# Kernel tuning notes

Measured on AMD Instinct MI355X. Metric: run time of the kernel, lower is better.

## Reference

```python
import jax, jax.numpy as jnp
import numpy as np

H = 64  # LSTM hidden size
IN = 5  # input feature size
N_ACTIONS = 3


def _init_params(key):
    ks = jax.random.split(key, 16)
    def u(k, shape, fan_in):
        b = 1.0 / np.sqrt(fan_in)
        return jax.random.uniform(k, shape, jnp.float32, -b, b)
    p = {}
    # PyTorch LSTM params: gate order i, f, g, o stacked along dim 0
    p['W_ih'] = u(ks[0], (4 * H, IN), H)
    p['W_hh'] = u(ks[1], (4 * H, H), H)
    p['b_ih'] = u(ks[2], (4 * H,), H)
    p['b_hh'] = u(ks[3], (4 * H,), H)
    p['W1'] = u(ks[4], (256, 64), 64); p['b1'] = u(ks[5], (256,), 64)
    p['W2'] = u(ks[6], (64, 256), 256); p['b2'] = u(ks[7], (64,), 256)
    p['W3'] = u(ks[8], (32, 64), 64); p['b3'] = u(ks[9], (32,), 64)
    p['W4'] = u(ks[10], (16, 32), 32); p['b4'] = u(ks[11], (16,), 32)
    p['Wh'] = u(ks[12], (N_ACTIONS, 16), 16); p['bh'] = u(ks[13], (N_ACTIONS,), 16)
    return p


def setup_inputs() -> dict:
    key = jax.random.key(0)
    k_x, k_h, k_c, k_p = jax.random.split(key, 4)
    B = 262144
    inp = {
        'x': jax.random.normal(k_x, (2, B, IN), jnp.float32),
        'h0': jax.random.normal(k_h, (B, H), jnp.float32),
        'c0': jax.random.normal(k_c, (B, H), jnp.float32),
    }
    inp.update(_init_params(k_p))
    return inp


def _lstm_step(x_t, h, c, W_ih, W_hh, b_ih, b_hh):
    # gates: [B, 4H], PyTorch order i, f, g, o
    gates = x_t @ W_ih.T + h @ W_hh.T + (b_ih + b_hh)
    i, f, g, o = jnp.split(gates, 4, axis=-1)
    i = jax.nn.sigmoid(i)
    f = jax.nn.sigmoid(f)
    g = jnp.tanh(g)
    o = jax.nn.sigmoid(o)
    c = f * c + i * g
    h = o * jnp.tanh(c)
    return h, c


def reference(x, h0, c0, W_ih, W_hh, b_ih, b_hh, W1, b1, W2, b2, W3, b3, W4, b4, Wh, bh):
    # 2-step LSTM (seq_len hard-coded to 2 in the torch module)
    h, c = h0, c0
    for t in range(2):
        h, c = _lstm_step(x[t], h, c, W_ih, W_hh, b_ih, b_hh)
    # take last timestep output, relu, then 4-layer MLP + head
    z = jax.nn.relu(h)
    z = jax.nn.relu(z @ W1.T + b1)
    z = jax.nn.relu(z @ W2.T + b2)
    z = jax.nn.relu(z @ W3.T + b3)
    z = jax.nn.relu(z @ W4.T + b4)
    return z @ Wh.T + bh
```

## Files before the change

kernel.cpp:

```cpp
#include <hip/hip_runtime.h>

typedef _Float16 f16;
typedef _Float16 f16x4 __attribute__((ext_vector_type(4)));
typedef _Float16 f16x8 __attribute__((ext_vector_type(8)));
typedef float    f32x4 __attribute__((ext_vector_type(4)));

__device__ __forceinline__ float sigmf(float x) {
    return __builtin_amdgcn_rcpf(1.0f + __expf(-x));
}
__device__ __forceinline__ float tanhf_fast(float x) {
    return 2.0f * sigmf(2.0f * x) - 1.0f;
}
#define MFMA(A,B,C) __builtin_amdgcn_mfma_f32_16x16x32_f16((A),(B),(C),0,0,0)

constexpr int STR = 72;

__global__ __launch_bounds__(512, 2)
void lstmdqn_v5(const float* __restrict__ xg,  const float* __restrict__ h0g,
                const float* __restrict__ c0g,
                const float* __restrict__ Wih, const float* __restrict__ Whh,
                const float* __restrict__ bih, const float* __restrict__ bhh,
                const float* __restrict__ w1p, const float* __restrict__ b1p,
                const float* __restrict__ w2p, const float* __restrict__ b2p,
                const float* __restrict__ w3p, const float* __restrict__ b3p,
                const float* __restrict__ w4p, const float* __restrict__ b4p,
                const float* __restrict__ whp, const float* __restrict__ bhp,
                float* __restrict__ out, int Bsz, int nt32) {
    __shared__ f16 sAB[256 * STR];
    __shared__ f16 sWG[9 * 256 * 8];
    __shared__ f16 sW1[8 * 256 * 8];
    __shared__ f16 sW2[32 * 64 * 8];
    __shared__ f16 sW3[8 * 32 * 8];
    __shared__ f16 sW4[4 * 16 * 8];
    __shared__ f16 sWh[4 * 16 * 8];
    __shared__ f16 sZL[2560];

    const int tid  = threadIdx.x;
    const int w    = tid >> 6, l = tid & 63;
    const int lrow = l & 15, hi = l >> 4;
    const int wrow = w * 32;

    for (int idx = tid; idx < 9 * 256 * 8; idx += 512) {
        int s = idx >> 11, n = (idx >> 3) & 255, j = idx & 7;
        float v;
        if (s < 8) v = Whh[n * 64 + s * 8 + j];
        else       v = (j < 5) ? Wih[n * 5 + j] : (j == 5 ? bih[n] + bhh[n] : 0.0f);
        sWG[idx] = (f16)v;
    }
    for (int idx = tid; idx < 8 * 256 * 8; idx += 512) {
        int s = idx >> 11, n = (idx >> 3) & 255, j = idx & 7;
        sW1[idx] = (f16)w1p[n * 64 + s * 8 + j];
    }
    for (int idx = tid; idx < 32 * 64 * 8; idx += 512) {
        int s = idx >> 9, n = (idx >> 3) & 63, j = idx & 7;
        sW2[idx] = (f16)w2p[n * 256 + s * 8 + j];
    }
    for (int idx = tid; idx < 8 * 32 * 8; idx += 512) {
        int s = idx >> 8, n = (idx >> 3) & 31, j = idx & 7;
        sW3[idx] = (f16)w3p[n * 64 + s * 8 + j];
    }
    for (int idx = tid; idx < 4 * 16 * 8; idx += 512) {
        int s = idx >> 7, n = (idx >> 3) & 15, j = idx & 7;
        sW4[idx] = (f16)w4p[n * 32 + s * 8 + j];
        int k = s * 8 + j;
        sWh[idx] = (f16)((k < 16 && n < 3) ? whp[n * 16 + k] : 0.0f);
    }
    for (int idx = tid; idx < 2560; idx += 512) sZL[idx] = (f16)0.0f;
    for (int idx = tid; idx < 256 * 3; idx += 512) {
        int r = idx / 3, c = 69 + (idx - 3 * r);
        sAB[r * STR + c] = (f16)(c == 69 ? 1.0f : 0.0f);
    }
    float bz1[16], bz2[4], bz3[2], bz4, bzh;
    #pragma unroll
    for (int ct = 0; ct < 16; ++ct) bz1[ct] = b1p[ct * 16 + lrow];
    #pragma unroll
    for (int ct = 0; ct < 4; ++ct)  bz2[ct] = b2p[ct * 16 + lrow];
    bz3[0] = b3p[lrow]; bz3[1] = b3p[16 + lrow];
    bz4 = b4p[lrow];
    bzh = (lrow < 3) ? bhp[lrow] : 0.0f;
    __syncthreads();

    const f16* pA[2]  = { &sAB[(wrow +  0 + lrow) * STR + hi * 8],
                          &sAB[(wrow + 16 + lrow) * STR + hi * 8] };
    const f16* pA2[2] = { (hi == 0) ? &sAB[(wrow +  0 + lrow) * STR + 64] : &sZL[l * 8],
                          (hi == 0) ? &sAB[(wrow + 16 + lrow) * STR + 64] : &sZL[l * 8] };
    const f16* pWG  = &sWG[(hi * 256 + lrow) * 8];
    const f16* pWG2 = (hi == 0) ? &sWG[8 * 2048 + lrow * 8] : &sZL[l * 8];
    const f16* pW1  = &sW1[(hi * 256 + lrow) * 8];
    const f16* pW2  = &sW2[(hi * 64 + lrow) * 8];
    const f16* pW3  = &sW3[(hi * 32 + lrow) * 8];
    const f16* pW4  = &sW4[(hi * 16 + lrow) * 8];
    const f16* pWh  = &sWh[(hi * 16 + lrow) * 8];
    int rowW[2][4];
    #pragma unroll
    for (int s = 0; s < 2; ++s)
        #pragma unroll
        for (int q = 0; q < 4; ++q)
            rowW[s][q] = (wrow + 16 * s + 4 * hi + q) * STR + lrow;

    #pragma unroll 1
    for (int tile = blockIdx.x * 8 + w; tile < nt32; tile += (gridDim.x << 3)) {
        const int rbase = tile * 32;

        {
            const float* hp = h0g + (size_t)rbase * 64;
            #pragma unroll
            for (int e = 0; e < 8; ++e) {
                float4 v = *(const float4*)(hp + e * 256 + l * 4);
                int r = wrow + 4 * e + (l >> 4);
                int col = (4 * l) & 63;
                f16x4 hv = { (f16)v.x, (f16)v.y, (f16)v.z, (f16)v.w };
                *(f16x4*)&sAB[r * STR + col] = hv;
            }
        }
        float creg[2][4][4];
        #pragma unroll
        for (int s = 0; s < 2; ++s)
            #pragma unroll
            for (int cg = 0; cg < 4; ++cg)
                #pragma unroll
                for (int q = 0; q < 4; ++q)
                    creg[s][cg][q] = c0g[(size_t)(rbase + 16 * s + 4 * hi + q) * 64 + cg * 16 + lrow];

        #pragma unroll
        for (int t = 0; t < 2; ++t) {
            if (l < 40) {
                const float* xp = xg + (size_t)t * Bsz * 5 + (size_t)rbase * 5;
                float4 v = *(const float4*)(xp + 4 * l);
                float vv[4] = { v.x, v.y, v.z, v.w };
                #pragma unroll
                for (int e = 0; e < 4; ++e) {
                    int idx = 4 * l + e, r = idx / 5, ft = idx - 5 * r;
                    sAB[(wrow + r) * STR + 64 + ft] = (f16)vv[e];
                }
            }
            f16x8 af0[2], af1[2], af2[2];
            #pragma unroll
            for (int s = 0; s < 2; ++s) {
                af0[s] = *(const f16x8*)&pA[s][0];
                af1[s] = *(const f16x8*)&pA[s][32];
                af2[s] = *(const f16x8*)pA2[s];
            }
            f32x4 acc[2][16];
            #pragma unroll
            for (int ct = 0; ct < 16; ++ct) {
                f16x8 b0 = *(const f16x8*)&pWG[ct * 128];
                f16x8 b1 = *(const f16x8*)&pWG[8192 + ct * 128];
                f16x8 b2 = *(const f16x8*)&pWG2[ct * 128];
                #pragma unroll
                for (int s = 0; s < 2; ++s) {
                    f32x4 a = { 0.f, 0.f, 0.f, 0.f };
                    a = MFMA(af0[s], b0, a);
                    a = MFMA(af1[s], b1, a);
                    a = MFMA(af2[s], b2, a);
                    acc[s][ct] = a;
                }
            }
            #pragma unroll
            for (int s = 0; s < 2; ++s)
                #pragma unroll
                for (int cg = 0; cg < 4; ++cg)
                    #pragma unroll
                    for (int q = 0; q < 4; ++q) {
                        float iv = sigmf(acc[s][cg][q]);
                        float fv = sigmf(acc[s][4 + cg][q]);
                        float gv = tanhf_fast(acc[s][8 + cg][q]);
                        float ov = sigmf(acc[s][12 + cg][q]);
                        float c  = fv * creg[s][cg][q] + iv * gv;
                        creg[s][cg][q] = c;
                        float h = ov * tanhf_fast(c);
                        if (t == 1) h = fmaxf(h, 0.0f);
                        sAB[rowW[s][q] + cg * 16] = (f16)h;
                    }
        }

        f16x8 za[2][2];
        #pragma unroll
        for (int s = 0; s < 2; ++s) {
            za[s][0] = *(const f16x8*)&pA[s][0];
            za[s][1] = *(const f16x8*)&pA[s][32];
        }
        f32x4 acc1[2][16];
        #pragma unroll
        for (int ct = 0; ct < 16; ++ct) {
            f16x8 b0 = *(const f16x8*)&pW1[ct * 128];
            f16x8 b1 = *(const f16x8*)&pW1[8192 + ct * 128];
            #pragma unroll
            for (int s = 0; s < 2; ++s) {
                f32x4 a = { 0.f, 0.f, 0.f, 0.f };
                a = MFMA(za[s][0], b0, a);
                a = MFMA(za[s][1], b1, a);
                acc1[s][ct] = a;
            }
        }
        f32x4 acc2[2][4];
        #pragma unroll
        for (int s = 0; s < 2; ++s)
            #pragma unroll
            for (int ct = 0; ct < 4; ++ct)
                acc2[s][ct] = (f32x4){ 0.f, 0.f, 0.f, 0.f };
        #pragma unroll
        for (int cc = 0; cc < 4; ++cc) {
            #pragma unroll
            for (int s = 0; s < 2; ++s)
                #pragma unroll
                for (int ctl = 0; ctl < 4; ++ctl)
                    #pragma unroll
                    for (int q = 0; q < 4; ++q) {
                        float v = fmaxf(acc1[s][cc * 4 + ctl][q] + bz1[cc * 4 + ctl], 0.0f);
                        sAB[rowW[s][q] + ctl * 16] = (f16)v;
                    }
            f16x8 ca[2][2];
            #pragma unroll
            for (int s = 0; s < 2; ++s) {
                ca[s][0] = *(const f16x8*)&pA[s][0];
                ca[s][1] = *(const f16x8*)&pA[s][32];
            }
            #pragma unroll
            for (int ct2 = 0; ct2 < 4; ++ct2) {
                f16x8 bb0 = *(const f16x8*)&pW2[cc * 4096 + ct2 * 128];
                f16x8 bb1 = *(const f16x8*)&pW2[cc * 4096 + 2048 + ct2 * 128];
                #pragma unroll
                for (int s = 0; s < 2; ++s) {
                    acc2[s][ct2] = MFMA(ca[s][0], bb0, acc2[s][ct2]);
                    acc2[s][ct2] = MFMA(ca[s][1], bb1, acc2[s][ct2]);
                }
            }
        }
        #pragma unroll
        for (int s = 0; s < 2; ++s)
            #pragma unroll
            for (int ct2 = 0; ct2 < 4; ++ct2)
                #pragma unroll
                for (int q = 0; q < 4; ++q) {
                    float v = fmaxf(acc2[s][ct2][q] + bz2[ct2], 0.0f);
                    sAB[rowW[s][q] + ct2 * 16] = (f16)v;
                }
        {
            f16x8 a3[2][2];
            #pragma unroll
            for (int s = 0; s < 2; ++s) {
                a3[s][0] = *(const f16x8*)&pA[s][0];
                a3[s][1] = *(const f16x8*)&pA[s][32];
            }
            f32x4 acc3[2][2];
            #pragma unroll
            for (int ctt = 0; ctt < 2; ++ctt) {
                f16x8 c0f = *(const f16x8*)&pW3[ctt * 128];
                f16x8 c1f = *(const f16x8*)&pW3[1024 + ctt * 128];
                #pragma unroll
                for (int s = 0; s < 2; ++s) {
                    f32x4 a = { 0.f, 0.f, 0.f, 0.f };
                    a = MFMA(a3[s][0], c0f, a);
                    a = MFMA(a3[s][1], c1f, a);
                    acc3[s][ctt] = a;
                }
            }
            #pragma unroll
            for (int s = 0; s < 2; ++s)
                #pragma unroll
                for (int ctt = 0; ctt < 2; ++ctt)
                    #pragma unroll
                    for (int q = 0; q < 4; ++q) {
                        float v = fmaxf(acc3[s][ctt][q] + bz3[ctt], 0.0f);
                        sAB[rowW[s][q] + ctt * 16] = (f16)v;
                    }
        }
        {
            f16x8 wb4 = *(const f16x8*)pW4;
            f32x4 acc4[2];
            #pragma unroll
            for (int s = 0; s < 2; ++s) {
                f16x8 a4 = *(const f16x8*)&pA[s][0];
                f32x4 a = { 0.f, 0.f, 0.f, 0.f };
                acc4[s] = MFMA(a4, wb4, a);
            }
            #pragma unroll
            for (int s = 0; s < 2; ++s)
                #pragma unroll
                for (int q = 0; q < 4; ++q) {
                    float v = fmaxf(acc4[s][q] + bz4, 0.0f);
                    sAB[rowW[s][q] + 32] = (f16)v;
                }
        }
        {
            f16x8 wbh = *(const f16x8*)pWh;
            f32x4 acch[2];
            #pragma unroll
            for (int s = 0; s < 2; ++s) {
                f16x8 ah = *(const f16x8*)&pA[s][32];
                f32x4 a = { 0.f, 0.f, 0.f, 0.f };
                acch[s] = MFMA(ah, wbh, a);
            }
            if (lrow < 3) {
                #pragma unroll
                for (int s = 0; s < 2; ++s)
                    #pragma unroll
                    for (int q = 0; q < 4; ++q)
                        out[(size_t)(rbase + 16 * s + 4 * hi + q) * 3 + lrow] = acch[s][q] + bzh;
            }
        }
    }
}

extern "C" void kernel_launch(void* const* d_in, const int* in_sizes, int n_in,
                              void* d_out, int out_size, void* d_ws, size_t ws_size,
                              hipStream_t stream) {
    const float* x   = (const float*)d_in[0];
    const float* h0  = (const float*)d_in[1];
    const float* c0  = (const float*)d_in[2];
    const float* Wih = (const float*)d_in[3];
    const float* Whh = (const float*)d_in[4];
    const float* bih = (const float*)d_in[5];
    const float* bhh = (const float*)d_in[6];
    const float* w1  = (const float*)d_in[7];
    const float* b1  = (const float*)d_in[8];
    const float* w2  = (const float*)d_in[9];
    const float* b2  = (const float*)d_in[10];
    const float* w3  = (const float*)d_in[11];
    const float* b3  = (const float*)d_in[12];
    const float* w4  = (const float*)d_in[13];
    const float* b4  = (const float*)d_in[14];
    const float* wh  = (const float*)d_in[15];
    const float* bh  = (const float*)d_in[16];

    int Bsz  = in_sizes[1] / 64;
    int nt32 = Bsz / 32;
    int grid = 256;

    lstmdqn_v5<<<grid, 512, 0, stream>>>(x, h0, c0, Wih, Whh, bih, bhh,
                                         w1, b1, w2, b2, w3, b3, w4, b4, wh, bh,
                                         (float*)d_out, Bsz, nt32);
}
```

Before: 92.66 us.

## Prepack weights in a prep kernel, read MLP weights from global, raise occupancy

Adds a separate kernel that converts and packs all weights to fp16 once per call, with the log2(e) factor folded into the gate weights so the activations can use exp2 directly. The main kernel keeps only the gate weights in shared memory and reads the MLP weights from global/L2, which cuts LDS use so four blocks can share a CU. Biases move from registers to shared memory. Gate and layer-1 accumulators are now processed in chunks to lower register pressure, and the grid doubles to 512. In exchange there is an extra launch, and MLP weight loads now come from global memory instead of LDS.

```diff
diff --git a/kernel.cpp b/kernel.cpp
--- a/kernel.cpp
+++ b/kernel.cpp
@@ -5,79 +5,93 @@
 typedef _Float16 f16x8 __attribute__((ext_vector_type(8)));
 typedef float    f32x4 __attribute__((ext_vector_type(4)));
 
-__device__ __forceinline__ float sigmf(float x) {
-    return __builtin_amdgcn_rcpf(1.0f + __expf(-x));
+#define MFMA(A,B,C) __builtin_amdgcn_mfma_f32_16x16x32_f16((A),(B),(C),0,0,0)
+
+__device__ __forceinline__ float sig2(float y) {
+    return __builtin_amdgcn_rcpf(1.0f + __builtin_amdgcn_exp2f(-y));
 }
-__device__ __forceinline__ float tanhf_fast(float x) {
-    return 2.0f * sigmf(2.0f * x) - 1.0f;
+
+constexpr float L2E  = 1.4426950408889634f;
+constexpr float L2E2 = 2.8853900817779268f;
+
+constexpr int STR = 72;
+
+constexpr int OFF_WG = 0;
+constexpr int OFF_W1 = 18432;
+constexpr int OFF_W2 = 34816;
+constexpr int OFF_W3 = 51200;
+constexpr int OFF_W4 = 53248;
+constexpr int OFF_WH = 53760;
+constexpr int WS_TOT = 54272;
+
+__global__ void wprep(const float* __restrict__ Wih, const float* __restrict__ Whh,
+                      const float* __restrict__ bih, const float* __restrict__ bhh,
+                      const float* __restrict__ w1p, const float* __restrict__ w2p,
+                      const float* __restrict__ w3p, const float* __restrict__ w4p,
+                      const float* __restrict__ whp, f16* __restrict__ ws) {
+    int idx = blockIdx.x * 256 + threadIdx.x;
+    if (idx >= WS_TOT) return;
+    float v = 0.0f;
+    if (idx < OFF_W1) {
+        int r = idx, kb = r >> 11, n = (r >> 3) & 255, j = r & 7;
+        float sc = (n >= 128 && n < 192) ? L2E2 : L2E;
+        if (kb < 8)      v = Whh[n * 64 + kb * 8 + j];
+        else if (j < 5)  v = Wih[n * 5 + j];
+        else if (j == 5) v = bih[n] + bhh[n];
+        v *= sc;
+    } else if (idx < OFF_W2) {
+        int r = idx - OFF_W1, kt = r >> 11, n = (r >> 3) & 255, j = r & 7;
+        v = w1p[n * 64 + kt * 8 + j];
+    } else if (idx < OFF_W3) {
+        int r = idx - OFF_W2, kt = r >> 9, n = (r >> 3) & 63, j = r & 7;
+        v = w2p[n * 256 + kt * 8 + j];
+    } else if (idx < OFF_W4) {
+        int r = idx - OFF_W3, kt = r >> 8, n = (r >> 3) & 31, j = r & 7;
+        v = w3p[n * 64 + kt * 8 + j];
+    } else if (idx < OFF_WH) {
+        int r = idx - OFF_W4, kt = r >> 7, n = (r >> 3) & 15, j = r & 7;
+        v = w4p[n * 32 + kt * 8 + j];
+    } else {
+        int r = idx - OFF_WH, kt = r >> 7, n = (r >> 3) & 15, j = r & 7;
+        int k = kt * 8 + j;
+        v = (k < 16 && n < 3) ? whp[n * 16 + k] : 0.0f;
+    }
+    ws[idx] = (f16)v;
 }
-#define MFMA(A,B,C) __builtin_amdgcn_mfma_f32_16x16x32_f16((A),(B),(C),0,0,0)
-
-constexpr int STR = 72;
-
-__global__ __launch_bounds__(512, 2)
-void lstmdqn_v5(const float* __restrict__ xg,  const float* __restrict__ h0g,
+
+__global__ __launch_bounds__(512, 4)
+void lstmdqn_v6(const float* __restrict__ xg,  const float* __restrict__ h0g,
                 const float* __restrict__ c0g,
-                const float* __restrict__ Wih, const float* __restrict__ Whh,
-                const float* __restrict__ bih, const float* __restrict__ bhh,
-                const float* __restrict__ w1p, const float* __restrict__ b1p,
-                const float* __restrict__ w2p, const float* __restrict__ b2p,
-                const float* __restrict__ w3p, const float* __restrict__ b3p,
-                const float* __restrict__ w4p, const float* __restrict__ b4p,
-                const float* __restrict__ whp, const float* __restrict__ bhp,
+                const f16* __restrict__ ws,
+                const float* __restrict__ b1p, const float* __restrict__ b2p,
+                const float* __restrict__ b3p, const float* __restrict__ b4p,
+                const float* __restrict__ bhp,
                 float* __restrict__ out, int Bsz, int nt32) {
     __shared__ f16 sAB[256 * STR];
     __shared__ f16 sWG[9 * 256 * 8];
-    __shared__ f16 sW1[8 * 256 * 8];
-    __shared__ f16 sW2[32 * 64 * 8];
-    __shared__ f16 sW3[8 * 32 * 8];
-    __shared__ f16 sW4[4 * 16 * 8];
-    __shared__ f16 sWh[4 * 16 * 8];
     __shared__ f16 sZL[2560];
+    __shared__ float sBB[372];
 
     const int tid  = threadIdx.x;
     const int w    = tid >> 6, l = tid & 63;
     const int lrow = l & 15, hi = l >> 4;
     const int wrow = w * 32;
 
-    for (int idx = tid; idx < 9 * 256 * 8; idx += 512) {
-        int s = idx >> 11, n = (idx >> 3) & 255, j = idx & 7;
-        float v;
-        if (s < 8) v = Whh[n * 64 + s * 8 + j];
-        else       v = (j < 5) ? Wih[n * 5 + j] : (j == 5 ? bih[n] + bhh[n] : 0.0f);
-        sWG[idx] = (f16)v;
+    {
+        const int4* src = (const int4*)(ws + OFF_WG);
+        int4* dst = (int4*)sWG;
+        for (int i = tid; i < 18432 / 8; i += 512) dst[i] = src[i];
     }
-    for (int idx = tid; idx < 8 * 256 * 8; idx += 512) {
-        int s = idx >> 11, n = (idx >> 3) & 255, j = idx & 7;
-        sW1[idx] = (f16)w1p[n * 64 + s * 8 + j];
-    }
-    for (int idx = tid; idx < 32 * 64 * 8; idx += 512) {
-        int s = idx >> 9, n = (idx >> 3) & 63, j = idx & 7;
-        sW2[idx] = (f16)w2p[n * 256 + s * 8 + j];
-    }
-    for (int idx = tid; idx < 8 * 32 * 8; idx += 512) {
-        int s = idx >> 8, n = (idx >> 3) & 31, j = idx & 7;
-        sW3[idx] = (f16)w3p[n * 64 + s * 8 + j];
-    }
-    for (int idx = tid; idx < 4 * 16 * 8; idx += 512) {
-        int s = idx >> 7, n = (idx >> 3) & 15, j = idx & 7;
-        sW4[idx] = (f16)w4p[n * 32 + s * 8 + j];
-        int k = s * 8 + j;
-        sWh[idx] = (f16)((k < 16 && n < 3) ? whp[n * 16 + k] : 0.0f);
-    }
-    for (int idx = tid; idx < 2560; idx += 512) sZL[idx] = (f16)0.0f;
-    for (int idx = tid; idx < 256 * 3; idx += 512) {
-        int r = idx / 3, c = 69 + (idx - 3 * r);
+    for (int i = tid; i < 2560; i += 512) sZL[i] = (f16)0.0f;
+    if (tid < 256) sBB[tid] = b1p[tid];
+    if (tid < 64)  sBB[256 + tid] = b2p[tid];
+    if (tid < 32)  sBB[320 + tid] = b3p[tid];
+    if (tid < 16)  sBB[352 + tid] = b4p[tid];
+    if (tid < 3)   sBB[368 + tid] = bhp[tid];
+    for (int i = tid; i < 256 * 3; i += 512) {
+        int r = i / 3, c = 69 + (i - 3 * r);
         sAB[r * STR + c] = (f16)(c == 69 ? 1.0f : 0.0f);
     }
-    float bz1[16], bz2[4], bz3[2], bz4, bzh;
-    #pragma unroll
-    for (int ct = 0; ct < 16; ++ct) bz1[ct] = b1p[ct * 16 + lrow];
-    #pragma unroll
-    for (int ct = 0; ct < 4; ++ct)  bz2[ct] = b2p[ct * 16 + lrow];
-    bz3[0] = b3p[lrow]; bz3[1] = b3p[16 + lrow];
-    bz4 = b4p[lrow];
-    bzh = (lrow < 3) ? bhp[lrow] : 0.0f;
     __syncthreads();
 
     const f16* pA[2]  = { &sAB[(wrow +  0 + lrow) * STR + hi * 8],
@@ -86,11 +100,11 @@
                           (hi == 0) ? &sAB[(wrow + 16 + lrow) * STR + 64] : &sZL[l * 8] };
     const f16* pWG  = &sWG[(hi * 256 + lrow) * 8];
     const f16* pWG2 = (hi == 0) ? &sWG[8 * 2048 + lrow * 8] : &sZL[l * 8];
-    const f16* pW1  = &sW1[(hi * 256 + lrow) * 8];
-    const f16* pW2  = &sW2[(hi * 64 + lrow) * 8];
-    const f16* pW3  = &sW3[(hi * 32 + lrow) * 8];
-    const f16* pW4  = &sW4[(hi * 16 + lrow) * 8];
-    const f16* pWh  = &sWh[(hi * 16 + lrow) * 8];
+    const f16* gW1 = ws + OFF_W1 + (hi * 256 + lrow) * 8;
+    const f16* gW2 = ws + OFF_W2 + (hi * 64 + lrow) * 8;
+    const f16* gW3 = ws + OFF_W3 + (hi * 32 + lrow) * 8;
+    const f16* gW4 = ws + OFF_W4 + (hi * 16 + lrow) * 8;
+    const f16* gWh = ws + OFF_WH + (hi * 16 + lrow) * 8;
     int rowW[2][4];
     #pragma unroll
     for (int s = 0; s < 2; ++s)
@@ -117,10 +131,10 @@
         #pragma unroll
         for (int s = 0; s < 2; ++s)
             #pragma unroll
-            for (int cg = 0; cg < 4; ++cg)
+            for (int gq = 0; gq < 4; ++gq)
                 #pragma unroll
                 for (int q = 0; q < 4; ++q)
-                    creg[s][cg][q] = c0g[(size_t)(rbase + 16 * s + 4 * hi + q) * 64 + cg * 16 + lrow];
+                    creg[s][gq][q] = c0g[(size_t)(rbase + 16 * s + 4 * hi + q) * 64 + gq * 16 + lrow];
 
         #pragma unroll
         for (int t = 0; t < 2; ++t) {
@@ -141,37 +155,40 @@
                 af1[s] = *(const f16x8*)&pA[s][32];
                 af2[s] = *(const f16x8*)pA2[s];
             }
-            f32x4 acc[2][16];
-            #pragma unroll
-            for (int ct = 0; ct < 16; ++ct) {
-                f16x8 b0 = *(const f16x8*)&pWG[ct * 128];
-                f16x8 b1 = *(const f16x8*)&pWG[8192 + ct * 128];
-                f16x8 b2 = *(const f16x8*)&pWG2[ct * 128];
-                #pragma unroll
-                for (int s = 0; s < 2; ++s) {
-                    f32x4 a = { 0.f, 0.f, 0.f, 0.f };
-                    a = MFMA(af0[s], b0, a);
-                    a = MFMA(af1[s], b1, a);
-                    a = MFMA(af2[s], b2, a);
-                    acc[s][ct] = a;
-                }
-            }
-            #pragma unroll
-            for (int s = 0; s < 2; ++s)
-                #pragma unroll
-                for (int cg = 0; cg < 4; ++cg)
+            #pragma unroll
+            for (int gq = 0; gq < 4; ++gq) {
+                f32x4 ag[4][2];
+                #pragma unroll
+                for (int g4 = 0; g4 < 4; ++g4) {
+                    int ct = gq + 4 * g4;
+                    f16x8 b0 = *(const f16x8*)&pWG[ct * 128];
+                    f16x8 b1 = *(const f16x8*)&pWG[8192 + ct * 128];
+                    f16x8 b2 = *(const f16x8*)&pWG2[ct * 128];
+                    #pragma unroll
+                    for (int s = 0; s < 2; ++s) {
+                        f32x4 a = { 0.f, 0.f, 0.f, 0.f };
+                        a = MFMA(af0[s], b0, a);
+                        a = MFMA(af1[s], b1, a);
+                        a = MFMA(af2[s], b2, a);
+                        ag[g4][s] = a;
+                    }
+                }
+                #pragma unroll
+                for (int s = 0; s < 2; ++s)
                     #pragma unroll
                     for (int q = 0; q < 4; ++q) {
-                        float iv = sigmf(acc[s][cg][q]);
-                        float fv = sigmf(acc[s][4 + cg][q]);
-                        float gv = tanhf_fast(acc[s][8 + cg][q]);
-                        float ov = sigmf(acc[s][12 + cg][q]);
-                        float c  = fv * creg[s][cg][q] + iv * gv;
-                        creg[s][cg][q] = c;
-                        float h = ov * tanhf_fast(c);
+                        float iv = sig2(ag[0][s][q]);
+                        float fv = sig2(ag[1][s][q]);
+                        float gv = 2.0f * sig2(ag[2][s][q]) - 1.0f;
+                        float ov = sig2(ag[3][s][q]);
+                        float c  = fv * creg[s][gq][q] + iv * gv;
+                        creg[s][gq][q] = c;
+                        float tc = 2.0f * sig2(L2E2 * c) - 1.0f;
+                        float h  = ov * tc;
                         if (t == 1) h = fmaxf(h, 0.0f);
-                        sAB[rowW[s][q] + cg * 16] = (f16)h;
+                        sAB[rowW[s][q] + gq * 16] = (f16)h;
                     }
+            }
         }
 
         f16x8 za[2][2];
@@ -180,36 +197,39 @@
             za[s][0] = *(const f16x8*)&pA[s][0];
             za[s][1] = *(const f16x8*)&pA[s][32];
         }
-        f32x4 acc1[2][16];
-        #pragma unroll
-        for (int ct = 0; ct < 16; ++ct) {
-            f16x8 b0 = *(const f16x8*)&pW1[ct * 128];
-            f16x8 b1 = *(const f16x8*)&pW1[8192 + ct * 128];
-            #pragma unroll
-            for (int s = 0; s < 2; ++s) {
-                f32x4 a = { 0.f, 0.f, 0.f, 0.f };
-                a = MFMA(za[s][0], b0, a);
-                a = MFMA(za[s][1], b1, a);
-                acc1[s][ct] = a;
-            }
-        }
         f32x4 acc2[2][4];
         #pragma unroll
         for (int s = 0; s < 2; ++s)
             #pragma unroll
-            for (int ct = 0; ct < 4; ++ct)
-                acc2[s][ct] = (f32x4){ 0.f, 0.f, 0.f, 0.f };
+            for (int c2 = 0; c2 < 4; ++c2)
+                acc2[s][c2] = (f32x4){ 0.f, 0.f, 0.f, 0.f };
         #pragma unroll
         for (int cc = 0; cc < 4; ++cc) {
-            #pragma unroll
-            for (int s = 0; s < 2; ++s)
-                #pragma unroll
-                for (int ctl = 0; ctl < 4; ++ctl)
+            f32x4 a1c[2][4];
+            #pragma unroll
+            for (int ctl = 0; ctl < 4; ++ctl) {
+                int ct = cc * 4 + ctl;
+                f16x8 b0 = *(const f16x8*)&gW1[ct * 128];
+                f16x8 b1 = *(const f16x8*)&gW1[8192 + ct * 128];
+                #pragma unroll
+                for (int s = 0; s < 2; ++s) {
+                    f32x4 a = { 0.f, 0.f, 0.f, 0.f };
+                    a = MFMA(za[s][0], b0, a);
+                    a = MFMA(za[s][1], b1, a);
+                    a1c[s][ctl] = a;
+                }
+            }
+            #pragma unroll
+            for (int ctl = 0; ctl < 4; ++ctl) {
+                float bv = sBB[(cc * 4 + ctl) * 16 + lrow];
+                #pragma unroll
+                for (int s = 0; s < 2; ++s)
                     #pragma unroll
                     for (int q = 0; q < 4; ++q) {
-                        float v = fmaxf(acc1[s][cc * 4 + ctl][q] + bz1[cc * 4 + ctl], 0.0f);
+                        float v = fmaxf(a1c[s][ctl][q] + bv, 0.0f);
                         sAB[rowW[s][q] + ctl * 16] = (f16)v;
                     }
+            }
             f16x8 ca[2][2];
             #pragma unroll
             for (int s = 0; s < 2; ++s) {
@@ -218,24 +238,26 @@
             }
             #pragma unroll
             for (int ct2 = 0; ct2 < 4; ++ct2) {
-                f16x8 bb0 = *(const f16x8*)&pW2[cc * 4096 + ct2 * 128];
-                f16x8 bb1 = *(const f16x8*)&pW2[cc * 4096 + 2048 + ct2 * 128];
+                f16x8 wb0 = *(const f16x8*)&gW2[cc * 4096 + ct2 * 128];
+                f16x8 wb1 = *(const f16x8*)&gW2[cc * 4096 + 2048 + ct2 * 128];
                 #pragma unroll
                 for (int s = 0; s < 2; ++s) {
-                    acc2[s][ct2] = MFMA(ca[s][0], bb0, acc2[s][ct2]);
-                    acc2[s][ct2] = MFMA(ca[s][1], bb1, acc2[s][ct2]);
-                }
-            }
-        }
-        #pragma unroll
-        for (int s = 0; s < 2; ++s)
-            #pragma unroll
-            for (int ct2 = 0; ct2 < 4; ++ct2)
+                    acc2[s][ct2] = MFMA(ca[s][0], wb0, acc2[s][ct2]);
+                    acc2[s][ct2] = MFMA(ca[s][1], wb1, acc2[s][ct2]);
+                }
+            }
+        }
+        #pragma unroll
+        for (int ct2 = 0; ct2 < 4; ++ct2) {
+            float bv = sBB[256 + ct2 * 16 + lrow];
+            #pragma unroll
+            for (int s = 0; s < 2; ++s)
                 #pragma unroll
                 for (int q = 0; q < 4; ++q) {
-                    float v = fmaxf(acc2[s][ct2][q] + bz2[ct2], 0.0f);
+                    float v = fmaxf(acc2[s][ct2][q] + bv, 0.0f);
                     sAB[rowW[s][q] + ct2 * 16] = (f16)v;
                 }
+        }
         {
             f16x8 a3[2][2];
             #pragma unroll
@@ -246,8 +268,8 @@
             f32x4 acc3[2][2];
             #pragma unroll
             for (int ctt = 0; ctt < 2; ++ctt) {
-                f16x8 c0f = *(const f16x8*)&pW3[ctt * 128];
-                f16x8 c1f = *(const f16x8*)&pW3[1024 + ctt * 128];
+                f16x8 c0f = *(const f16x8*)&gW3[ctt * 128];
+                f16x8 c1f = *(const f16x8*)&gW3[1024 + ctt * 128];
                 #pragma unroll
                 for (int s = 0; s < 2; ++s) {
                     f32x4 a = { 0.f, 0.f, 0.f, 0.f };
@@ -257,47 +279,45 @@
                 }
             }
             #pragma unroll
-            for (int s = 0; s < 2; ++s)
-                #pragma unroll
-                for (int ctt = 0; ctt < 2; ++ctt)
+            for (int ctt = 0; ctt < 2; ++ctt) {
+                float bv = sBB[320 + ctt * 16 + lrow];
+                #pragma unroll
+                for (int s = 0; s < 2; ++s)
                     #pragma unroll
                     for (int q = 0; q < 4; ++q) {
-                        float v = fmaxf(acc3[s][ctt][q] + bz3[ctt], 0.0f);
+                        float v = fmaxf(acc3[s][ctt][q] + bv, 0.0f);
                         sAB[rowW[s][q] + ctt * 16] = (f16)v;
                     }
+            }
         }
         {
-            f16x8 wb4 = *(const f16x8*)pW4;
-            f32x4 acc4[2];
+            f16x8 wb4 = *(const f16x8*)gW4;
+            float bv = sBB[352 + lrow];
             #pragma unroll
             for (int s = 0; s < 2; ++s) {
                 f16x8 a4 = *(const f16x8*)&pA[s][0];
                 f32x4 a = { 0.f, 0.f, 0.f, 0.f };
-                acc4[s] = MFMA(a4, wb4, a);
-            }
-            #pragma unroll
-            for (int s = 0; s < 2; ++s)
+                a = MFMA(a4, wb4, a);
                 #pragma unroll
                 for (int q = 0; q < 4; ++q) {
-                    float v = fmaxf(acc4[s][q] + bz4, 0.0f);
+                    float v = fmaxf(a[q] + bv, 0.0f);
                     sAB[rowW[s][q] + 32] = (f16)v;
                 }
+            }
         }
         {
-            f16x8 wbh = *(const f16x8*)pWh;
-            f32x4 acch[2];
+            f16x8 wbh = *(const f16x8*)gWh;
             #pragma unroll
             for (int s = 0; s < 2; ++s) {
                 f16x8 ah = *(const f16x8*)&pA[s][32];
                 f32x4 a = { 0.f, 0.f, 0.f, 0.f };
-                acch[s] = MFMA(ah, wbh, a);
-            }
-            if (lrow < 3) {
-                #pragma unroll
-                for (int s = 0; s < 2; ++s)
+                a = MFMA(ah, wbh, a);
+                if (lrow < 3) {
+                    float bv = sBB[368 + lrow];
                     #pragma unroll
                     for (int q = 0; q < 4; ++q)
-                        out[(size_t)(rbase + 16 * s + 4 * hi + q) * 3 + lrow] = acch[s][q] + bzh;
+                        out[(size_t)(rbase + 16 * s + 4 * hi + q) * 3 + lrow] = a[q] + bv;
+                }
             }
         }
     }
@@ -326,9 +346,10 @@
 
     int Bsz  = in_sizes[1] / 64;
     int nt32 = Bsz / 32;
-    int grid = 256;
-
-    lstmdqn_v5<<<grid, 512, 0, stream>>>(x, h0, c0, Wih, Whh, bih, bhh,
-                                         w1, b1, w2, b2, w3, b3, w4, b4, wh, bh,
-                                         (float*)d_out, Bsz, nt32);
+
+    f16* ws = (f16*)d_ws;
+    wprep<<<(WS_TOT + 255) / 256, 256, 0, stream>>>(Wih, Whh, bih, bhh,
+                                                    w1, w2, w3, w4, wh, ws);
+    lstmdqn_v6<<<512, 512, 0, stream>>>(x, h0, c0, ws, b1, b2, b3, b4, bh,
+                                        (float*)d_out, Bsz, nt32);
 }
```

Result: slower. 244.1 us (+163.4%).
